# Kernel tuning notes

Measured on AMD Instinct MI355X. Metric: run time of the kernel, lower is better.

The kernel has to match this reference:

```python
import jax, jax.numpy as jnp
import numpy as np

N = 50000      # num nodes
C_IN = 128     # channels[0]
C_OUT = 128    # channels[1]
D = 16         # fixed node degree
T = 4          # diffusion steps
H_MLP = 64     # diff_mlp hidden
H_GRU = 128    # GRUAggr hidden
EPS = 0.01


def setup_inputs() -> dict:
    key = jax.random.key(0)
    ks = jax.random.split(key, 10)
    node_attr = jax.random.normal(ks[0], (N, C_IN), jnp.float32)
    # adjacency sorted by source: node i owns columns [i*D, i*D+D)
    src = jnp.repeat(jnp.arange(N), D)
    dst = jax.random.randint(ks[1], (N * D,), 0, N)
    edge_index = jnp.stack([src, dst])                       # [2, N*D]
    slices = jnp.stack([jnp.arange(N) * D, jnp.full((N,), D)], axis=1)  # [N,2] (start,count)
    noise = EPS * jax.random.normal(ks[2], (T, N, D), jnp.float32)      # eps*randn per step
    init = lambda k, shape, fan: (jax.random.normal(k, shape, jnp.float32) / np.sqrt(fan))
    W1 = init(ks[3], ((1 + T) * C_IN, H_MLP), (1 + T) * C_IN)
    b1 = jnp.zeros((H_MLP,), jnp.float32)
    W2 = init(ks[4], (H_MLP, 1), H_MLP)
    b2 = jnp.zeros((1,), jnp.float32)
    Wx = init(ks[5], (C_IN, 3 * H_GRU), C_IN)
    Wh = init(ks[6], (H_GRU, 3 * H_GRU), H_GRU)
    bx = jnp.zeros((3 * H_GRU,), jnp.float32)
    bh = jnp.zeros((3 * H_GRU,), jnp.float32)
    Wo = init(ks[7], (H_GRU, C_OUT), H_GRU)
    bo = jnp.zeros((C_OUT,), jnp.float32)
    return dict(node_attr=node_attr, edge_index=edge_index, slices=slices, noise=noise,
                W1=W1, b1=b1, W2=W2, b2=b2, Wx=Wx, Wh=Wh, bx=bx, bh=bh, Wo=Wo, bo=bo)


def _gru(x_seq, Wx, Wh, bx, bh):
    # x_seq: [T+1, N, C]; torch GRU gate order (r, z, n)
    H = Wh.shape[0]
    def step(h, x):
        gx = x @ Wx + bx
        gh = h @ Wh + bh
        xr, xz, xn = jnp.split(gx, 3, axis=-1)
        hr, hz, hn = jnp.split(gh, 3, axis=-1)
        r = jax.nn.sigmoid(xr + hr)
        z = jax.nn.sigmoid(xz + hz)
        n = jnp.tanh(xn + r * hn)
        return (1.0 - z) * n + z * h, None
    h0 = jnp.zeros((x_seq.shape[1], H), x_seq.dtype)
    h, _ = jax.lax.scan(step, h0, x_seq)
    return h


def reference(node_attr, edge_index, slices, noise, W1, b1, W2, b2, Wx, Wh, bx, bh, Wo, bo):
    n, C = node_attr.shape
    t_steps, _, deg = noise.shape
    dst = edge_index[1]
    walk_embeds = jnp.zeros((n, 1 + t_steps, C), node_attr.dtype).at[:, 0, :].set(node_attr)
    cur = jnp.arange(n)
    for t in range(t_steps):
        starts = slices[cur, 0]                              # slice_cat(adj, adj_slic_t)
        nbr = dst[starts[:, None] + jnp.arange(deg)]         # [N, D] neighbor node ids
        v_t = node_attr[nbr]                                 # [N, D, C]
        # diff_mlp on [prefix walk embed | candidate neighbor]: split the first
        # linear layer so the shared prefix is computed once per node (position
        # 1+t of walk_embeds is still zero, matching the original fill order).
        h_pre = walk_embeds.reshape(n, (1 + t_steps) * C) @ W1 + b1       # [N, H_MLP]
        h_nbr = jnp.einsum('ndc,ch->ndh', v_t, W1[(1 + t) * C:(2 + t) * C])
        logp = (jax.nn.relu(h_pre[:, None, :] + h_nbr) @ W2)[..., 0] + b2[0]  # [N, D]
        logp = jax.lax.stop_gradient(logp)                   # torch.no_grad()
        # scatter_logsumexp over init node == logsumexp over the D candidates
        p = jnp.exp(logp - jax.nn.logsumexp(logp, axis=1, keepdims=True)) + noise[t]
        sel = jnp.argmax(p, axis=1)                          # scatter_max per init node
        cur = nbr[jnp.arange(n), sel]                        # walks_t
        walk_embeds = walk_embeds.at[:, 1 + t, :].set(node_attr[cur])
    h = _gru(jnp.transpose(walk_embeds, (1, 0, 2)), Wx, Wh, bx, bh)
    return h @ Wo + bo                                       # [N, C_OUT]
```

## Files before the change

### kernel.cpp

```cpp
#include <hip/hip_runtime.h>
#include <math.h>

#define NND 50000
#define DEG 16

typedef __attribute__((ext_vector_type(8))) short short8v;
typedef __attribute__((ext_vector_type(4))) float float4v;

#define OFF_HPRE 0ULL
#define OFF_PROJ 12800000ULL
#define OFF_XB   64000000ULL
#define OFF_IDX  102400000ULL
#define OFF_BQF  103600384ULL
#define OFF_WOF  103862528ULL
#define WS_NEED  103895296ULL

#define LOG2E 1.44269504088896f

__device__ __forceinline__ float fast_sig(float x){
    return __builtin_amdgcn_rcpf(1.f + __builtin_amdgcn_exp2f(-LOG2E*x));
}
__device__ __forceinline__ float fast_tanh(float x){
    return fmaf(-2.f, __builtin_amdgcn_rcpf(1.f + __builtin_amdgcn_exp2f((2.f*LOG2E)*x)), 1.f);
}
__device__ __forceinline__ unsigned short f2bf(float f){
    unsigned int u = __float_as_uint(f);
    u += 0x7FFFu + ((u >> 16) & 1u);
    return (unsigned short)(u >> 16);
}
__device__ __forceinline__ float bf2f(unsigned short h){
    return __uint_as_float(((unsigned int)h) << 16);
}

__global__ __launch_bounds__(256) void k_iota(int* __restrict__ idx0){
    int i = blockIdx.x*256 + threadIdx.x;
    if (i < NND) idx0[i] = i;
}

__global__ __launch_bounds__(256) void k_projall(const float* __restrict__ A,
    const float* __restrict__ W1, const float* __restrict__ b1,
    float* __restrict__ hpre, float* __restrict__ proj)
{
    __shared__ float Al[64][33];
    __shared__ float Bl[32][68];
    const int tid = threadIdx.x;
    const int row0 = blockIdx.x << 6;
    const int y = blockIdx.y;
    const float* B = W1 + (size_t)y*128*64;
    const int row_t = tid >> 4, col_t = tid & 15;
    float4 acc[4];
#pragma unroll
    for (int i=0;i<4;i++) acc[i] = make_float4(0.f,0.f,0.f,0.f);
    for (int k0 = 0; k0 < 128; k0 += 32){
#pragma unroll
        for (int r=0;r<2;r++){
            int am = (tid>>3) + (r<<5);
            int ak = (tid&7) << 2;
            int gr = row0 + am; if (gr >= NND) gr = NND-1;
            float4 v = *(const float4*)(A + (size_t)gr*128 + k0 + ak);
            Al[am][ak] = v.x; Al[am][ak+1] = v.y; Al[am][ak+2] = v.z; Al[am][ak+3] = v.w;
        }
#pragma unroll
        for (int r=0;r<2;r++){
            int p = (r<<8) + tid;
            int bk = p >> 4, bc = (p & 15) << 2;
            *(float4*)(&Bl[bk][bc]) = *(const float4*)(B + (size_t)(k0+bk)*64 + bc);
        }
        __syncthreads();
#pragma unroll 8
        for (int k=0;k<32;k++){
            float4 b = *(const float4*)(&Bl[k][col_t<<2]);
#pragma unroll
            for (int i=0;i<4;i++){
                float a = Al[(row_t<<2)+i][k];
                acc[i].x = fmaf(a, b.x, acc[i].x);
                acc[i].y = fmaf(a, b.y, acc[i].y);
                acc[i].z = fmaf(a, b.z, acc[i].z);
                acc[i].w = fmaf(a, b.w, acc[i].w);
            }
        }
        __syncthreads();
    }
    float4 bb = make_float4(0.f,0.f,0.f,0.f);
    if (y == 0) bb = *(const float4*)(b1 + (col_t<<2));
    float* dst = (y == 0) ? hpre : (proj + (size_t)(y-1)*NND*64);
#pragma unroll
    for (int i=0;i<4;i++){
        int gr = row0 + (row_t<<2) + i;
        if (gr < NND){
            float4 o = make_float4(acc[i].x+bb.x, acc[i].y+bb.y, acc[i].z+bb.z, acc[i].w+bb.w);
            *(float4*)(dst + (size_t)gr*64 + (col_t<<2)) = o;
        }
    }
}

__global__ __launch_bounds__(256) void k_walk4(
    const float* __restrict__ hpre0, const float* __restrict__ proj,
    const int* __restrict__ dst, const float* __restrict__ W2,
    const float* __restrict__ b2, const float* __restrict__ noise,
    int* __restrict__ idxb)
{
    const int tid = threadIdx.x;
    const int sg = tid >> 4, l = tid & 15;
    const int gi = (blockIdx.x << 4) + sg;
    float4 hp = *(const float4*)(hpre0 + ((size_t)gi<<6) + (l<<2));
    float4 w2 = *(const float4*)(W2 + (l<<2));
    const float b2s = b2[0];
    int curv = gi;
#pragma unroll 1
    for (int t=0; t<4; t++){
        const float* pj = proj + (size_t)t*NND*64;
        const int nbr = dst[curv*DEG + l];
        float4 val[16];
#pragma unroll
        for (int d=0; d<16; d++){
            int nd = __shfl(nbr, d, 16);
            val[d] = *(const float4*)(pj + ((size_t)nd<<6) + (l<<2));
        }
        float lp = 0.f;
#pragma unroll
        for (int d=0; d<16; d++){
            float4 v = val[d];
            float q =  fmaxf(hp.x+v.x,0.f)*w2.x;
            q = fmaf(fmaxf(hp.y+v.y,0.f), w2.y, q);
            q = fmaf(fmaxf(hp.z+v.z,0.f), w2.z, q);
            q = fmaf(fmaxf(hp.w+v.w,0.f), w2.w, q);
            q += __shfl_xor(q, 1, 16);
            q += __shfl_xor(q, 2, 16);
            q += __shfl_xor(q, 4, 16);
            q += __shfl_xor(q, 8, 16);
            if (l == d) lp = q + b2s;
        }
        float mx = lp;
#pragma unroll
        for (int off=8; off; off>>=1) mx = fmaxf(mx, __shfl_xor(mx, off, 16));
        float s = expf(lp - mx);
#pragma unroll
        for (int off=8; off; off>>=1) s += __shfl_xor(s, off, 16);
        float p = expf(lp - mx - logf(s)) + noise[(size_t)t*NND*DEG + ((size_t)gi<<4) + l];
        float bv = p; int bi = l;
#pragma unroll
        for (int off=8; off; off>>=1){
            float ov = __shfl_xor(bv, off, 16);
            int   oi = __shfl_xor(bi, off, 16);
            if (ov > bv || (ov == bv && oi < bi)){ bv = ov; bi = oi; }
        }
        int sel = __shfl(nbr, bi, 16);
        if (l == 0) idxb[(size_t)(t+1)*NND + gi] = sel;
        float4 u = *(const float4*)(pj + ((size_t)sel<<6) + (l<<2));
        hp.x += u.x; hp.y += u.y; hp.z += u.z; hp.w += u.w;
        curv = sel;
    }
}

__global__ __launch_bounds__(256) void k_pack_x(const float* __restrict__ na,
    unsigned short* __restrict__ Xb)
{
    int i = blockIdx.x*256 + threadIdx.x;
    if (i < NND*32){
        float4 v = *(const float4*)(na + (size_t)i*4);
        unsigned long long pk = (unsigned long long)f2bf(v.x)
            | ((unsigned long long)f2bf(v.y) << 16)
            | ((unsigned long long)f2bf(v.z) << 32)
            | ((unsigned long long)f2bf(v.w) << 48);
        *(unsigned long long*)(Xb + (size_t)i*4) = pk;
    }
}

__global__ __launch_bounds__(256) void k_pack_bqf(const float* __restrict__ Wx,
    const float* __restrict__ Wh, unsigned short* __restrict__ BqF)
{
    int i = blockIdx.x*256 + threadIdx.x;
    int jj = i & 7, lane = (i>>3)&63, ct = (i>>9)&7, c = (i>>12)&7, y = i>>15;
    int g = ct>>1, jh = ct&1, mm = lane&15, quad = lane>>4;
    int jg = (y<<5) + (jh<<4) + mm;
    int k = (c<<5) + (quad<<3) + jj;
    float v = 0.f;
    if (k < 128){
        if (g < 3) v = Wh[k*384 + g*128 + jg];
    } else {
        int kk = k - 128;
        if (g == 0)      v = Wx[kk*384 + jg];
        else if (g == 1) v = Wx[kk*384 + 128 + jg];
        else if (g == 3) v = Wx[kk*384 + 256 + jg];
    }
    BqF[i] = f2bf(v);
}

__global__ __launch_bounds__(256) void k_pack_wof(const float* __restrict__ Wo,
    unsigned short* __restrict__ WoF)
{
    int i = blockIdx.x*256 + threadIdx.x;
    int jj = i & 7, lane = (i>>3)&63, ct = (i>>9)&7, c = i>>12;
    int n = (ct<<4) + (lane&15);
    int k = (c<<5) + ((lane>>4)<<3) + jj;
    WoF[i] = f2bf(Wo[k*128 + n]);
}

__global__ __launch_bounds__(256,2) void k_gru5(
    const unsigned short* __restrict__ Xb,
    const unsigned short* __restrict__ BqF,
    const unsigned short* __restrict__ WoF,
    const float* __restrict__ bx, const float* __restrict__ bh,
    const float* __restrict__ bo, const int* __restrict__ idxb,
    float* __restrict__ out)
{
    __shared__ unsigned short A_l[8192];
    __shared__ unsigned short X_l[16384];
    const int tid = threadIdx.x;
    const int w = tid >> 6, lane = tid & 63;
    const int m = lane & 15, quad = lane >> 4;
    const int row0 = blockIdx.x << 6;
    const int r = tid & 63, q = tid >> 6;
    int gr = row0 + r; if (gr >= NND) gr = NND-1;
    const int rt_s = r >> 4, m_s = r & 15;
    float brr[2], bzz[2], bxn[2], bhn[2];
#pragma unroll
    for (int jh=0; jh<2; jh++){
        int j = (w<<5) + (jh<<4) + m;
        brr[jh] = bx[j] + bh[j];
        bzz[jh] = bx[128+j] + bh[128+j];
        bxn[jh] = bx[256+j];
        bhn[jh] = bh[256+j];
    }
    unsigned short holdv[2][4][4];
    short8v xv[4];
    {
        const int xr = idxb[gr];
        const unsigned short* xrow = Xb + (size_t)xr*128 + (q<<5);
#pragma unroll
        for (int u=0;u<4;u++) xv[u] = *(const short8v*)(xrow + (u<<3));
#pragma unroll
        for (int u=0;u<4;u++)
            *(short8v*)(X_l + (((rt_s<<2)+q)*64 + (u<<4) + m_s)*8) = xv[u];
        const int xr1 = idxb[NND + gr];
        const unsigned short* xrow1 = Xb + (size_t)xr1*128 + (q<<5);
#pragma unroll
        for (int u=0;u<4;u++) xv[u] = *(const short8v*)(xrow1 + (u<<3));
    }
    __syncthreads();

#pragma unroll 1
    for (int s=0; s<5; s++){
        const unsigned short* Xcur = X_l + ((s&1)<<13);
        float4v zero = {0.f,0.f,0.f,0.f};
        float4v acc[32];
#pragma unroll
        for (int i=0;i<32;i++) acc[i] = zero;
        const int c0 = (s == 0) ? 4 : 0;
        for (int c=c0;c<8;c++){
            const unsigned short* asrc = (c < 4) ? A_l : Xcur;
            short8v afr[4];
#pragma unroll
            for (int rt=0;rt<4;rt++)
                afr[rt] = *(const short8v*)(asrc + (((rt<<2) + (c&3))*64 + lane)*8);
            const unsigned short* bp = BqF + ((((size_t)w*8 + c)*8)*64 + lane)*8;
#pragma unroll
            for (int ct=0;ct<8;ct++){
                short8v bf = *(const short8v*)(bp + (ct<<9));
#pragma unroll
                for (int rt=0;rt<4;rt++)
                    acc[(ct<<2)+rt] = __builtin_amdgcn_mfma_f32_16x16x32_bf16(afr[rt], bf, acc[(ct<<2)+rt], 0,0,0);
            }
        }
        if (s < 4){
            unsigned short* Xnxt = X_l + (((s+1)&1)<<13);
#pragma unroll
            for (int u=0;u<4;u++)
                *(short8v*)(Xnxt + (((rt_s<<2)+q)*64 + (u<<4) + m_s)*8) = xv[u];
            if (s < 3){
                const int xr = idxb[(size_t)(s+2)*NND + gr];
                const unsigned short* xrow = Xb + (size_t)xr*128 + (q<<5);
#pragma unroll
                for (int u=0;u<4;u++) xv[u] = *(const short8v*)(xrow + (u<<3));
            }
        }
#pragma unroll
        for (int jh=0; jh<2; jh++){
#pragma unroll
            for (int rt=0; rt<4; rt++){
#pragma unroll
                for (int r4=0; r4<4; r4++){
                    float rg = fast_sig(acc[(jh<<2)+rt][r4] + brr[jh]);
                    float zg = fast_sig(acc[((2+jh)<<2)+rt][r4] + bzz[jh]);
                    float ng = fast_tanh(acc[((6+jh)<<2)+rt][r4] + bxn[jh] + rg*(acc[((4+jh)<<2)+rt][r4] + bhn[jh]));
                    float hold = (s == 0) ? 0.f : bf2f(holdv[jh][rt][r4]);
                    holdv[jh][rt][r4] = f2bf((1.f - zg)*ng + zg*hold);
                }
            }
        }
        __syncthreads();
#pragma unroll
        for (int jh=0; jh<2; jh++)
#pragma unroll
            for (int rt=0; rt<4; rt++)
#pragma unroll
                for (int r4=0; r4<4; r4++){
                    int ha = ((((rt<<2)+w)*64 + (((jh<<1)+(m>>3))<<4) + (quad<<2)+r4)<<3) + (m&7);
                    A_l[ha] = holdv[jh][rt][r4];
                }
        __syncthreads();
    }
    float4v zero = {0.f,0.f,0.f,0.f};
    float4v acco[8];
#pragma unroll
    for (int i=0;i<8;i++) acco[i] = zero;
    for (int c=0;c<4;c++){
        short8v afr[4];
#pragma unroll
        for (int rt=0;rt<4;rt++)
            afr[rt] = *(const short8v*)(A_l + (((rt<<2) + c)*64 + lane)*8);
#pragma unroll
        for (int cto=0;cto<2;cto++){
            short8v bf = *(const short8v*)(WoF + (((size_t)(c*8 + (w<<1)+cto))*64 + lane)*8);
#pragma unroll
            for (int rt=0;rt<4;rt++)
                acco[(cto<<2)+rt] = __builtin_amdgcn_mfma_f32_16x16x32_bf16(afr[rt], bf, acco[(cto<<2)+rt], 0,0,0);
        }
    }
#pragma unroll
    for (int cto=0; cto<2; cto++){
        int col = (w<<5) + (cto<<4) + m;
        float bb = bo[col];
#pragma unroll
        for (int rt=0; rt<4; rt++){
#pragma unroll
            for (int r4=0; r4<4; r4++){
                int row = row0 + (rt<<4) + (quad<<2) + r4;
                if (row < NND) out[(size_t)row*128 + col] = acco[(cto<<2)+rt][r4] + bb;
            }
        }
    }
}

extern "C" void kernel_launch(void* const* d_in, const int* in_sizes, int n_in,
                              void* d_out, int out_size, void* d_ws, size_t ws_size,
                              hipStream_t stream)
{
    const float* node_attr = (const float*)d_in[0];
    const int*   edge_index= (const int*)  d_in[1];
    const float* noise = (const float*)d_in[3];
    const float* W1 = (const float*)d_in[4];
    const float* b1 = (const float*)d_in[5];
    const float* W2 = (const float*)d_in[6];
    const float* b2 = (const float*)d_in[7];
    const float* Wx = (const float*)d_in[8];
    const float* Wh = (const float*)d_in[9];
    const float* bx = (const float*)d_in[10];
    const float* bh = (const float*)d_in[11];
    const float* Wo = (const float*)d_in[12];
    const float* bo = (const float*)d_in[13];
    const int* dst = edge_index + (size_t)NND*DEG;
    float* out = (float*)d_out;
    if (ws_size < WS_NEED) return;

    char* ws = (char*)d_ws;
    float* hpre = (float*)(ws + OFF_HPRE);
    float* proj = (float*)(ws + OFF_PROJ);
    unsigned short* Xb  = (unsigned short*)(ws + OFF_XB);
    int* idxb = (int*)(ws + OFF_IDX);
    unsigned short* BqF = (unsigned short*)(ws + OFF_BQF);
    unsigned short* WoF = (unsigned short*)(ws + OFF_WOF);

    k_iota<<<dim3(196), dim3(256), 0, stream>>>(idxb);
    k_pack_x  <<<dim3(6250), dim3(256), 0, stream>>>(node_attr, Xb);
    k_pack_bqf<<<dim3(512),  dim3(256), 0, stream>>>(Wx, Wh, BqF);
    k_pack_wof<<<dim3(64),   dim3(256), 0, stream>>>(Wo, WoF);

    k_projall<<<dim3(782, 5), dim3(256), 0, stream>>>(node_attr, W1, b1, hpre, proj);
    k_walk4<<<dim3(3125), dim3(256), 0, stream>>>(hpre, proj, dst, W2, b2, noise, idxb);

    k_gru5<<<dim3(782), dim3(256), 0, stream>>>(Xb, BqF, WoF, bx, bh, bo, idxb, out);
}
```

Before: 382.8 us.

## Compute all five W1 projections per block from one A tile load

The projection kernel now processes all five 128x64 W1 slices in a single block instead of one slice per grid-y index. Each A row tile is loaded once and reused across the five outputs, and A is stored transposed in shared memory so it can be read with vector loads. This cuts redundant global reads of node_attr and issues fewer blocks, but raises per-thread register use (80 accumulators) and shared memory. The GRU kernel's launch bound is also raised to 3 blocks per SM to push occupancy, which may force register spills.

```diff
diff --git a/kernel.cpp b/kernel.cpp
--- a/kernel.cpp
+++ b/kernel.cpp
@@ -41,55 +41,65 @@
     const float* __restrict__ W1, const float* __restrict__ b1,
     float* __restrict__ hpre, float* __restrict__ proj)
 {
-    __shared__ float Al[64][33];
-    __shared__ float Bl[32][68];
+    __shared__ float Alt[32][68];
+    __shared__ float Bl[5][32][64];
     const int tid = threadIdx.x;
     const int row0 = blockIdx.x << 6;
-    const int y = blockIdx.y;
-    const float* B = W1 + (size_t)y*128*64;
     const int row_t = tid >> 4, col_t = tid & 15;
-    float4 acc[4];
-#pragma unroll
-    for (int i=0;i<4;i++) acc[i] = make_float4(0.f,0.f,0.f,0.f);
+    float4 acc[4][5];
+#pragma unroll
+    for (int i=0;i<4;i++)
+#pragma unroll
+        for (int y=0;y<5;y++) acc[i][y] = make_float4(0.f,0.f,0.f,0.f);
+
     for (int k0 = 0; k0 < 128; k0 += 32){
-#pragma unroll
-        for (int r=0;r<2;r++){
-            int am = (tid>>3) + (r<<5);
-            int ak = (tid&7) << 2;
-            int gr = row0 + am; if (gr >= NND) gr = NND-1;
-            float4 v = *(const float4*)(A + (size_t)gr*128 + k0 + ak);
-            Al[am][ak] = v.x; Al[am][ak+1] = v.y; Al[am][ak+2] = v.z; Al[am][ak+3] = v.w;
-        }
-#pragma unroll
-        for (int r=0;r<2;r++){
-            int p = (r<<8) + tid;
-            int bk = p >> 4, bc = (p & 15) << 2;
-            *(float4*)(&Bl[bk][bc]) = *(const float4*)(B + (size_t)(k0+bk)*64 + bc);
+        {
+            int row = tid >> 2, kq = tid & 3;
+            int gr = row0 + row; if (gr >= NND) gr = NND-1;
+            const float* ap = A + (size_t)gr*128 + k0 + (kq<<3);
+            float4 v0 = *(const float4*)(ap);
+            float4 v1 = *(const float4*)(ap + 4);
+            int kb = kq<<3;
+            Alt[kb+0][row] = v0.x; Alt[kb+1][row] = v0.y; Alt[kb+2][row] = v0.z; Alt[kb+3][row] = v0.w;
+            Alt[kb+4][row] = v1.x; Alt[kb+5][row] = v1.y; Alt[kb+6][row] = v1.z; Alt[kb+7][row] = v1.w;
+        }
+#pragma unroll
+        for (int i=0;i<10;i++){
+            int p = (i<<8) + tid;
+            int y = p >> 9, rem = p & 511;
+            ((float4*)Bl)[p] = ((const float4*)(W1 + ((size_t)y*128 + k0)*64))[rem];
         }
         __syncthreads();
-#pragma unroll 8
+#pragma unroll 4
         for (int k=0;k<32;k++){
-            float4 b = *(const float4*)(&Bl[k][col_t<<2]);
-#pragma unroll
-            for (int i=0;i<4;i++){
-                float a = Al[(row_t<<2)+i][k];
-                acc[i].x = fmaf(a, b.x, acc[i].x);
-                acc[i].y = fmaf(a, b.y, acc[i].y);
-                acc[i].z = fmaf(a, b.z, acc[i].z);
-                acc[i].w = fmaf(a, b.w, acc[i].w);
+            float4 av = *(const float4*)(&Alt[k][row_t<<2]);
+            float aa[4] = {av.x, av.y, av.z, av.w};
+#pragma unroll
+            for (int y=0;y<5;y++){
+                float4 bv = *(const float4*)(&Bl[y][k][col_t<<2]);
+#pragma unroll
+                for (int i=0;i<4;i++){
+                    acc[i][y].x = fmaf(aa[i], bv.x, acc[i][y].x);
+                    acc[i][y].y = fmaf(aa[i], bv.y, acc[i][y].y);
+                    acc[i][y].z = fmaf(aa[i], bv.z, acc[i][y].z);
+                    acc[i][y].w = fmaf(aa[i], bv.w, acc[i][y].w);
+                }
             }
         }
         __syncthreads();
     }
-    float4 bb = make_float4(0.f,0.f,0.f,0.f);
-    if (y == 0) bb = *(const float4*)(b1 + (col_t<<2));
-    float* dst = (y == 0) ? hpre : (proj + (size_t)(y-1)*NND*64);
-#pragma unroll
-    for (int i=0;i<4;i++){
-        int gr = row0 + (row_t<<2) + i;
-        if (gr < NND){
-            float4 o = make_float4(acc[i].x+bb.x, acc[i].y+bb.y, acc[i].z+bb.z, acc[i].w+bb.w);
-            *(float4*)(dst + (size_t)gr*64 + (col_t<<2)) = o;
+    float4 bb = *(const float4*)(b1 + (col_t<<2));
+#pragma unroll
+    for (int y=0;y<5;y++){
+        float* dstp = (y==0) ? hpre : (proj + (size_t)(y-1)*NND*64);
+#pragma unroll
+        for (int i=0;i<4;i++){
+            int gr = row0 + (row_t<<2) + i;
+            if (gr < NND){
+                float4 o = acc[i][y];
+                if (y==0){ o.x+=bb.x; o.y+=bb.y; o.z+=bb.z; o.w+=bb.w; }
+                *(float4*)(dstp + ((size_t)gr<<6) + (col_t<<2)) = o;
+            }
         }
     }
 }
@@ -197,7 +207,7 @@
     WoF[i] = f2bf(Wo[k*128 + n]);
 }
 
-__global__ __launch_bounds__(256,2) void k_gru5(
+__global__ __launch_bounds__(256,3) void k_gru5(
     const unsigned short* __restrict__ Xb,
     const unsigned short* __restrict__ BqF,
     const unsigned short* __restrict__ WoF,
@@ -367,7 +377,7 @@
     k_pack_bqf<<<dim3(512),  dim3(256), 0, stream>>>(Wx, Wh, BqF);
     k_pack_wof<<<dim3(64),   dim3(256), 0, stream>>>(Wo, WoF);
 
-    k_projall<<<dim3(782, 5), dim3(256), 0, stream>>>(node_attr, W1, b1, hpre, proj);
+    k_projall<<<dim3(782), dim3(256), 0, stream>>>(node_attr, W1, b1, hpre, proj);
     k_walk4<<<dim3(3125), dim3(256), 0, stream>>>(hpre, proj, dst, W2, b2, noise, idxb);
 
     k_gru5<<<dim3(782), dim3(256), 0, stream>>>(Xb, BqF, WoF, bx, bh, bo, idxb, out);
```

After: 519.1 us. +35.6%, slower.
